# Performance work log

Measured on AMD Instinct MI355X. Metric: run time of the kernel, lower is better.

## Reference

```python
import jax, jax.numpy as jnp
import numpy as np

H, I, E, TOPK = 1024, 4096, 8, 2
B, S = 2, 2048


def setup_inputs() -> dict:
    key = jax.random.key(0)
    ks = jax.random.split(key, 6)
    x = jax.random.normal(ks[0], (B, S, H), dtype=jnp.float32)
    expert_indices = jax.random.randint(ks[1], (B, S, TOPK), 0, E)
    expert_weights = jax.random.uniform(ks[2], (B, S, TOPK), dtype=jnp.float32)
    gate_proj = jax.random.normal(ks[3], (E, I, H), dtype=jnp.float32) * 0.02
    up_proj = jax.random.normal(ks[4], (E, I, H), dtype=jnp.float32) * 0.02
    down_proj = jax.random.normal(ks[5], (E, H, I), dtype=jnp.float32) * 0.02
    return {"x": x, "expert_indices": expert_indices, "expert_weights": expert_weights,
            "gate_proj": gate_proj, "up_proj": up_proj, "down_proj": down_proj}


def reference(x, expert_indices, expert_weights, gate_proj, up_proj, down_proj):
    b, s, h = x.shape
    xf = x.reshape(-1, h)                      # [T, H]
    ei = expert_indices.reshape(-1, expert_indices.shape[-1])   # [T, K]
    ew = expert_weights.reshape(-1, expert_weights.shape[-1])   # [T, K]
    n_experts = gate_proj.shape[0]
    out = jnp.zeros_like(xf)
    for e in range(n_experts):
        # combined routing weight of this expert per token (sum over topk slots)
        w_e = jnp.sum(jnp.where(ei == e, ew, 0.0), axis=-1)     # [T]
        g = xf @ gate_proj[e].T                # [T, I]
        u = xf @ up_proj[e].T                  # [T, I]
        inter = jax.nn.silu(g) * u             # fused SiLU*mul
        out = out + w_e[:, None] * (inter @ down_proj[e].T)     # weighted scatter-add
    return out.reshape(b, s, h)
```

## Files before the change

### kernel.cpp

```cpp
#include <hip/hip_runtime.h>
#include <cstdint>
#include <cstddef>

#define H_DIM 1024
#define I_DIM 4096
#define E_NUM 8
#define TOPK  2
#define T_NUM 4096
#define NROWS (T_NUM * TOPK)
#define BK    64

typedef _Float16 half8 __attribute__((ext_vector_type(8)));
typedef float    f32x4 __attribute__((ext_vector_type(4)));

__device__ __forceinline__ void async_copy16(void* lds, const void* g)
{
    __builtin_amdgcn_global_load_lds(
        (__attribute__((address_space(1))) unsigned int*)g,
        (__attribute__((address_space(3))) unsigned int*)lds,
        16 , 0 , 0 );
}


#define NX4 (T_NUM * H_DIM / 4)
#define NW4 (E_NUM * I_DIM * H_DIM / 4)
__global__ void cvt_all(const float* __restrict__ x,  const float* __restrict__ gp,
                        const float* __restrict__ up, const float* __restrict__ dp,
                        _Float16* __restrict__ xh, _Float16* __restrict__ wg,
                        _Float16* __restrict__ wu, _Float16* __restrict__ wd)
{
    int i = blockIdx.x * blockDim.x + threadIdx.x;
    const int total = NX4 + 3 * NW4;
    if (i >= total) return;
    const float* s; _Float16* d; int j;
    if (i < NX4)              { s = x;  d = xh; j = i; }
    else if (i < NX4 + NW4)   { s = gp; d = wg; j = i - NX4; }
    else if (i < NX4 + 2*NW4) { s = up; d = wu; j = i - NX4 - NW4; }
    else                      { s = dp; d = wd; j = i - NX4 - 2*NW4; }
    float4 v = reinterpret_cast<const float4*>(s)[j];
    union { _Float16 h[4]; unsigned long long u; } o;
    o.h[0] = (_Float16)v.x; o.h[1] = (_Float16)v.y;
    o.h[2] = (_Float16)v.z; o.h[3] = (_Float16)v.w;
    reinterpret_cast<unsigned long long*>(d)[j] = o.u;
}

__global__ void route_all(const int* __restrict__ ei, const float* __restrict__ ew,
                          int* __restrict__ offs,
                          int* __restrict__ token_of_row, float* __restrict__ weight_of_row)
{
    __shared__ int cnt[E_NUM];
    __shared__ int cur[E_NUM];
    const int t = (int)threadIdx.x;
    if (t < E_NUM) cnt[t] = 0;
    __syncthreads();
    for (int s = t; s < NROWS; s += (int)blockDim.x) atomicAdd(&cnt[ei[s]], 1);
    __syncthreads();
    if (t == 0) {
        int acc = 0;
        for (int e = 0; e < E_NUM; ++e) { offs[e] = acc; cur[e] = acc; acc += cnt[e]; }
        offs[E_NUM] = acc;
    }
    __syncthreads();
    for (int s = t; s < NROWS; s += (int)blockDim.x) {
        int e = ei[s];
        int r = atomicAdd(&cur[e], 1);
        token_of_row[r]  = s >> 1;
        weight_of_row[r] = ew[s];
    }
}

__global__ __launch_bounds__(256, 3) void gateup_gemm(
    const _Float16* __restrict__ xh,
    const _Float16* __restrict__ Wg,
    const _Float16* __restrict__ Wu,
    const int*      __restrict__ token_of_row,
    const int*      __restrict__ offs,
    _Float16*       __restrict__ inter)
{
    const int e = blockIdx.z;
    const int seg_start = offs[e], seg_end = offs[e + 1];
    const int m0 = seg_start + (int)blockIdx.y * 128;
    if (m0 >= seg_end) return;
    const int n0 = (int)blockIdx.x * 64;

    __shared__ _Float16 Ash[128 * BK];
    __shared__ _Float16 Bgs[64 * BK];
    __shared__ _Float16 Bus[64 * BK];

    const int tid  = (int)threadIdx.x;
    const int lane = tid & 63, wid = tid >> 6;
    const int wm = wid >> 1, wn = wid & 1;

    const int r8 = lane >> 3;
    const int c8 = lane & 7;
    const int gc = c8 ^ r8;

    const _Float16* pA[4];
    _Float16* lA[4];
#pragma unroll
    for (int j = 0; j < 4; ++j) {
        int q = 4 * wid + j;
        int r = m0 + q * 8 + r8;
        if (r > seg_end - 1) r = seg_end - 1;
        int tok = token_of_row[r];
        pA[j] = xh + (size_t)tok * H_DIM + gc * 8;
        lA[j] = &Ash[q * 8 * BK];
    }
    const _Float16* pBg[2]; const _Float16* pBu[2];
    _Float16* lBg[2]; _Float16* lBu[2];
#pragma unroll
    for (int j = 0; j < 2; ++j) {
        int q = 2 * wid + j;
        int row = q * 8 + r8;
        pBg[j] = Wg + ((size_t)e * I_DIM + n0 + row) * H_DIM + gc * 8;
        pBu[j] = Wu + ((size_t)e * I_DIM + n0 + row) * H_DIM + gc * 8;
        lBg[j] = &Bgs[q * 8 * BK];
        lBu[j] = &Bus[q * 8 * BK];
    }

    f32x4 accg[4][2], accu[4][2];
#pragma unroll
    for (int i = 0; i < 4; ++i)
#pragma unroll
        for (int j = 0; j < 2; ++j) {
            accg[i][j] = (f32x4){0.f, 0.f, 0.f, 0.f};
            accu[i][j] = (f32x4){0.f, 0.f, 0.f, 0.f};
        }

    const int fm = lane & 15, kq = lane >> 4;
    const int f3 = fm & 7;

    constexpr int NK = H_DIM / BK;
    for (int kt = 0; kt < NK; ++kt) {
        const int ko = kt * BK;
        __syncthreads();
#pragma unroll
        for (int j = 0; j < 4; ++j) async_copy16(lA[j], pA[j] + ko);
#pragma unroll
        for (int j = 0; j < 2; ++j) {
            async_copy16(lBg[j], pBg[j] + ko);
            async_copy16(lBu[j], pBu[j] + ko);
        }
        __syncthreads();

#pragma unroll
        for (int h = 0; h < 2; ++h) {
            const int rdo = (((h << 2) | kq) ^ f3) * 8;
            half8 a[4], bg[2], bu[2];
#pragma unroll
            for (int i = 0; i < 4; ++i)
                a[i] = *(const half8*)&Ash[(wm * 64 + i * 16 + fm) * BK + rdo];
#pragma unroll
            for (int j = 0; j < 2; ++j) {
                bg[j] = *(const half8*)&Bgs[(wn * 32 + j * 16 + fm) * BK + rdo];
                bu[j] = *(const half8*)&Bus[(wn * 32 + j * 16 + fm) * BK + rdo];
            }
#pragma unroll
            for (int i = 0; i < 4; ++i)
#pragma unroll
                for (int j = 0; j < 2; ++j) {
                    accg[i][j] = __builtin_amdgcn_mfma_f32_16x16x32_f16(a[i], bg[j], accg[i][j], 0, 0, 0);
                    accu[i][j] = __builtin_amdgcn_mfma_f32_16x16x32_f16(a[i], bu[j], accu[i][j], 0, 0, 0);
                }
        }
    }

#pragma unroll
    for (int i = 0; i < 4; ++i) {
#pragma unroll
        for (int reg = 0; reg < 4; ++reg) {
            int r = m0 + wm * 64 + i * 16 + kq * 4 + reg;
            if (r < seg_end) {
#pragma unroll
                for (int j = 0; j < 2; ++j) {
                    int col = n0 + wn * 32 + j * 16 + fm;
                    float g = accg[i][j][reg];
                    float u = accu[i][j][reg];
                    float sv = (g / (1.f + __expf(-g))) * u;
                    inter[(size_t)r * I_DIM + col] = (_Float16)sv;
                }
            }
        }
    }
}

__global__ __launch_bounds__(256, 3) void down_gemm(
    const _Float16* __restrict__ inter,
    const _Float16* __restrict__ Wd,
    const int*      __restrict__ token_of_row,
    const float*    __restrict__ weight_of_row,
    const int*      __restrict__ offs,
    float*          __restrict__ out)
{
    const int e = blockIdx.z;
    const int seg_start = offs[e], seg_end = offs[e + 1];
    const int m0 = seg_start + (int)blockIdx.y * 128;
    if (m0 >= seg_end) return;
    const int n0 = (int)blockIdx.x * 128;

    __shared__ _Float16 Ash[128 * BK];
    __shared__ _Float16 Bsh[128 * BK];

    const int tid  = (int)threadIdx.x;
    const int lane = tid & 63, wid = tid >> 6;
    const int wm = wid >> 1, wn = wid & 1;
    const int r8 = lane >> 3;
    const int c8 = lane & 7;
    const int gc = c8 ^ r8;

    const _Float16* pA[4]; _Float16* lA[4];
    const _Float16* pB[4]; _Float16* lB[4];
#pragma unroll
    for (int j = 0; j < 4; ++j) {
        int q = 4 * wid + j;
        int row_in = q * 8 + r8;
        int r = m0 + row_in;
        if (r > seg_end - 1) r = seg_end - 1;
        pA[j] = inter + (size_t)r * I_DIM + gc * 8;
        lA[j] = &Ash[q * 8 * BK];
        int n = n0 + row_in;
        pB[j] = Wd + ((size_t)e * H_DIM + n) * I_DIM + gc * 8;
        lB[j] = &Bsh[q * 8 * BK];
    }

    f32x4 acc[4][4];
#pragma unroll
    for (int i = 0; i < 4; ++i)
#pragma unroll
        for (int j = 0; j < 4; ++j) acc[i][j] = (f32x4){0.f, 0.f, 0.f, 0.f};

    const int fm = lane & 15, kq = lane >> 4;
    const int f3 = fm & 7;

    constexpr int NK = I_DIM / BK;
    for (int kt = 0; kt < NK; ++kt) {
        const int ko = kt * BK;
        __syncthreads();
#pragma unroll
        for (int j = 0; j < 4; ++j) {
            async_copy16(lA[j], pA[j] + ko);
            async_copy16(lB[j], pB[j] + ko);
        }
        __syncthreads();

#pragma unroll
        for (int h = 0; h < 2; ++h) {
            const int rdo = (((h << 2) | kq) ^ f3) * 8;
            half8 a[4], b[4];
#pragma unroll
            for (int i = 0; i < 4; ++i)
                a[i] = *(const half8*)&Ash[(wm * 64 + i * 16 + fm) * BK + rdo];
#pragma unroll
            for (int j = 0; j < 4; ++j)
                b[j] = *(const half8*)&Bsh[(wn * 64 + j * 16 + fm) * BK + rdo];
#pragma unroll
            for (int i = 0; i < 4; ++i)
#pragma unroll
                for (int j = 0; j < 4; ++j)
                    acc[i][j] = __builtin_amdgcn_mfma_f32_16x16x32_f16(a[i], b[j], acc[i][j], 0, 0, 0);
        }
    }

#pragma unroll
    for (int i = 0; i < 4; ++i) {
#pragma unroll
        for (int reg = 0; reg < 4; ++reg) {
            int r = m0 + wm * 64 + i * 16 + kq * 4 + reg;
            if (r < seg_end) {
                float w = weight_of_row[r];
                int   t = token_of_row[r];
#pragma unroll
                for (int j = 0; j < 4; ++j) {
                    int col = n0 + wn * 64 + j * 16 + fm;
                    atomicAdd(&out[(size_t)t * H_DIM + col], w * acc[i][j][reg]);
                }
            }
        }
    }
}

extern "C" void kernel_launch(void* const* d_in, const int* in_sizes, int n_in,
                              void* d_out, int out_size, void* d_ws, size_t ws_size,
                              hipStream_t stream)
{
    const float* x  = (const float*)d_in[0];
    const int*   ei = (const int*)  d_in[1];
    const float* ew = (const float*)d_in[2];
    const float* gp = (const float*)d_in[3];
    const float* up = (const float*)d_in[4];
    const float* dp = (const float*)d_in[5];
    float* out = (float*)d_out;

    char* ws = (char*)d_ws;
    size_t o = 0;
    _Float16* xh    = (_Float16*)(ws + o); o += (size_t)T_NUM * H_DIM * 2;
    _Float16* Wg_h  = (_Float16*)(ws + o); o += (size_t)E_NUM * I_DIM * H_DIM * 2;
    _Float16* Wu_h  = (_Float16*)(ws + o); o += (size_t)E_NUM * I_DIM * H_DIM * 2;
    _Float16* Wd_h  = (_Float16*)(ws + o); o += (size_t)E_NUM * I_DIM * H_DIM * 2;
    _Float16* inter = (_Float16*)(ws + o); o += (size_t)NROWS * I_DIM * 2;
    int*   offs          = (int*)  (ws + o);
    int*   token_of_row  = (int*)  (ws + o + 256);
    float* weight_of_row = (float*)(ws + o + 256 + (size_t)NROWS * 4);
    size_t ws_need = o + 256 + (size_t)NROWS * 8;
    if (ws_size < ws_need) return;

    hipMemsetAsync(d_out, 0, (size_t)out_size * sizeof(float), stream);

    const int nt = 256;
    const int ncvt = NX4 + 3 * NW4;
    cvt_all<<<(ncvt + nt - 1) / nt, nt, 0, stream>>>(x, gp, up, dp, xh, Wg_h, Wu_h, Wd_h);

    route_all<<<1, 1024, 0, stream>>>(ei, ew, offs, token_of_row, weight_of_row);

    gateup_gemm<<<dim3(I_DIM / 64, NROWS / 128, E_NUM), 256, 0, stream>>>(
        xh, Wg_h, Wu_h, token_of_row, offs, inter);
    down_gemm<<<dim3(H_DIM / 128, NROWS / 128, E_NUM), 256, 0, stream>>>(
        inter, Wd_h, token_of_row, weight_of_row, offs, out);
}
```

Before: 685.9 us.

## Persistent-style M loops in MoE GEMMs, 512-thread gate/up tiles, fold output zeroing

The gate/up GEMM now uses 512 threads with 256-row M tiles, and each block loops over M tiles with a fixed y-grid instead of launching one block per worst-case tile. The down GEMM gets a similar grid-stride loop over M tiles with a fixed y extent. The conversion kernel becomes grid-stride with 2048 blocks and also zeroes the output, replacing the separate memset. The intent is to cut the many empty blocks launched for the worst-case row count, raise B-tile reuse, and drop one launch. The risks are load imbalance across the fixed y-blocks and lower occupancy from the larger blocks and shared memory.

```diff
diff --git a/kernel.cpp b/kernel.cpp
--- a/kernel.cpp
+++ b/kernel.cpp
@@ -27,21 +27,25 @@
 __global__ void cvt_all(const float* __restrict__ x,  const float* __restrict__ gp,
                         const float* __restrict__ up, const float* __restrict__ dp,
                         _Float16* __restrict__ xh, _Float16* __restrict__ wg,
-                        _Float16* __restrict__ wu, _Float16* __restrict__ wd)
-{
-    int i = blockIdx.x * blockDim.x + threadIdx.x;
+                        _Float16* __restrict__ wu, _Float16* __restrict__ wd,
+                        float* __restrict__ out)
+{
     const int total = NX4 + 3 * NW4;
-    if (i >= total) return;
-    const float* s; _Float16* d; int j;
-    if (i < NX4)              { s = x;  d = xh; j = i; }
-    else if (i < NX4 + NW4)   { s = gp; d = wg; j = i - NX4; }
-    else if (i < NX4 + 2*NW4) { s = up; d = wu; j = i - NX4 - NW4; }
-    else                      { s = dp; d = wd; j = i - NX4 - 2*NW4; }
-    float4 v = reinterpret_cast<const float4*>(s)[j];
-    union { _Float16 h[4]; unsigned long long u; } o;
-    o.h[0] = (_Float16)v.x; o.h[1] = (_Float16)v.y;
-    o.h[2] = (_Float16)v.z; o.h[3] = (_Float16)v.w;
-    reinterpret_cast<unsigned long long*>(d)[j] = o.u;
+    const int nth = (int)(gridDim.x * blockDim.x);
+    for (int i = (int)(blockIdx.x * blockDim.x + threadIdx.x); i < total; i += nth) {
+        const float* s; _Float16* d; int j;
+        if (i < NX4)              { s = x;  d = xh; j = i; }
+        else if (i < NX4 + NW4)   { s = gp; d = wg; j = i - NX4; }
+        else if (i < NX4 + 2*NW4) { s = up; d = wu; j = i - NX4 - NW4; }
+        else                      { s = dp; d = wd; j = i - NX4 - 2*NW4; }
+        float4 v = reinterpret_cast<const float4*>(s)[j];
+        union { _Float16 h[4]; unsigned long long u; } o;
+        o.h[0] = (_Float16)v.x; o.h[1] = (_Float16)v.y;
+        o.h[2] = (_Float16)v.z; o.h[3] = (_Float16)v.w;
+        reinterpret_cast<unsigned long long*>(d)[j] = o.u;
+    }
+    for (int i = (int)(blockIdx.x * blockDim.x + threadIdx.x); i < T_NUM * H_DIM / 4; i += nth)
+        reinterpret_cast<float4*>(out)[i] = (float4){0.f, 0.f, 0.f, 0.f};
 }
 
 __global__ void route_all(const int* __restrict__ ei, const float* __restrict__ ew,
@@ -69,7 +73,8 @@
     }
 }
 
-__global__ __launch_bounds__(256, 3) void gateup_gemm(
+#define GUP_Y 6
+__global__ __launch_bounds__(512) void gateup_gemm(
     const _Float16* __restrict__ xh,
     const _Float16* __restrict__ Wg,
     const _Float16* __restrict__ Wu,
@@ -79,11 +84,9 @@
 {
     const int e = blockIdx.z;
     const int seg_start = offs[e], seg_end = offs[e + 1];
-    const int m0 = seg_start + (int)blockIdx.y * 128;
-    if (m0 >= seg_end) return;
     const int n0 = (int)blockIdx.x * 64;
 
-    __shared__ _Float16 Ash[128 * BK];
+    __shared__ _Float16 Ash[256 * BK];
     __shared__ _Float16 Bgs[64 * BK];
     __shared__ _Float16 Bus[64 * BK];
 
@@ -95,95 +98,89 @@
     const int c8 = lane & 7;
     const int gc = c8 ^ r8;
 
-    const _Float16* pA[4];
-    _Float16* lA[4];
-#pragma unroll
-    for (int j = 0; j < 4; ++j) {
-        int q = 4 * wid + j;
-        int r = m0 + q * 8 + r8;
-        if (r > seg_end - 1) r = seg_end - 1;
-        int tok = token_of_row[r];
-        pA[j] = xh + (size_t)tok * H_DIM + gc * 8;
-        lA[j] = &Ash[q * 8 * BK];
-    }
-    const _Float16* pBg[2]; const _Float16* pBu[2];
-    _Float16* lBg[2]; _Float16* lBu[2];
-#pragma unroll
-    for (int j = 0; j < 2; ++j) {
-        int q = 2 * wid + j;
-        int row = q * 8 + r8;
-        pBg[j] = Wg + ((size_t)e * I_DIM + n0 + row) * H_DIM + gc * 8;
-        pBu[j] = Wu + ((size_t)e * I_DIM + n0 + row) * H_DIM + gc * 8;
-        lBg[j] = &Bgs[q * 8 * BK];
-        lBu[j] = &Bus[q * 8 * BK];
-    }
-
-    f32x4 accg[4][2], accu[4][2];
-#pragma unroll
-    for (int i = 0; i < 4; ++i)
-#pragma unroll
-        for (int j = 0; j < 2; ++j) {
-            accg[i][j] = (f32x4){0.f, 0.f, 0.f, 0.f};
-            accu[i][j] = (f32x4){0.f, 0.f, 0.f, 0.f};
-        }
-
     const int fm = lane & 15, kq = lane >> 4;
     const int f3 = fm & 7;
 
-    constexpr int NK = H_DIM / BK;
-    for (int kt = 0; kt < NK; ++kt) {
-        const int ko = kt * BK;
-        __syncthreads();
-#pragma unroll
-        for (int j = 0; j < 4; ++j) async_copy16(lA[j], pA[j] + ko);
-#pragma unroll
-        for (int j = 0; j < 2; ++j) {
-            async_copy16(lBg[j], pBg[j] + ko);
-            async_copy16(lBu[j], pBu[j] + ko);
-        }
-        __syncthreads();
-
-#pragma unroll
-        for (int h = 0; h < 2; ++h) {
-            const int rdo = (((h << 2) | kq) ^ f3) * 8;
-            half8 a[4], bg[2], bu[2];
-#pragma unroll
-            for (int i = 0; i < 4; ++i)
-                a[i] = *(const half8*)&Ash[(wm * 64 + i * 16 + fm) * BK + rdo];
+    for (int yb = (int)blockIdx.y; seg_start + yb * 256 < seg_end; yb += GUP_Y) {
+        const int m0 = seg_start + yb * 256;
+
+        const _Float16* pA[4]; int oA[4];
+#pragma unroll
+        for (int j = 0; j < 4; ++j) {
+            int q = 4 * wid + j;
+            int r = m0 + q * 8 + r8;
+            if (r > seg_end - 1) r = seg_end - 1;
+            int tok = token_of_row[r];
+            pA[j] = xh + (size_t)tok * H_DIM + gc * 8;
+            oA[j] = q * 8 * BK;
+        }
+        const int brow = wid * 8 + r8;
+        const _Float16* pBg = Wg + ((size_t)e * I_DIM + n0 + brow) * H_DIM + gc * 8;
+        const _Float16* pBu = Wu + ((size_t)e * I_DIM + n0 + brow) * H_DIM + gc * 8;
+        const int oB = wid * 8 * BK;
+
+        f32x4 accg[4][2], accu[4][2];
+#pragma unroll
+        for (int i = 0; i < 4; ++i)
 #pragma unroll
             for (int j = 0; j < 2; ++j) {
-                bg[j] = *(const half8*)&Bgs[(wn * 32 + j * 16 + fm) * BK + rdo];
-                bu[j] = *(const half8*)&Bus[(wn * 32 + j * 16 + fm) * BK + rdo];
-            }
-#pragma unroll
-            for (int i = 0; i < 4; ++i)
+                accg[i][j] = (f32x4){0.f, 0.f, 0.f, 0.f};
+                accu[i][j] = (f32x4){0.f, 0.f, 0.f, 0.f};
+            }
+
+        constexpr int NK = H_DIM / BK;
+        for (int kt = 0; kt < NK; ++kt) {
+            const int ko = kt * BK;
+            __syncthreads();
+#pragma unroll
+            for (int j = 0; j < 4; ++j) async_copy16(&Ash[oA[j]], pA[j] + ko);
+            async_copy16(&Bgs[oB], pBg + ko);
+            async_copy16(&Bus[oB], pBu + ko);
+            __syncthreads();
+
+#pragma unroll
+            for (int h = 0; h < 2; ++h) {
+                const int rdo = (((h << 2) | kq) ^ f3) * 8;
+                half8 a[4], bg[2], bu[2];
+#pragma unroll
+                for (int i = 0; i < 4; ++i)
+                    a[i] = *(const half8*)&Ash[(wm * 64 + i * 16 + fm) * BK + rdo];
 #pragma unroll
                 for (int j = 0; j < 2; ++j) {
-                    accg[i][j] = __builtin_amdgcn_mfma_f32_16x16x32_f16(a[i], bg[j], accg[i][j], 0, 0, 0);
-                    accu[i][j] = __builtin_amdgcn_mfma_f32_16x16x32_f16(a[i], bu[j], accu[i][j], 0, 0, 0);
+                    bg[j] = *(const half8*)&Bgs[(wn * 32 + j * 16 + fm) * BK + rdo];
+                    bu[j] = *(const half8*)&Bus[(wn * 32 + j * 16 + fm) * BK + rdo];
                 }
-        }
-    }
-
-#pragma unroll
-    for (int i = 0; i < 4; ++i) {
-#pragma unroll
-        for (int reg = 0; reg < 4; ++reg) {
-            int r = m0 + wm * 64 + i * 16 + kq * 4 + reg;
-            if (r < seg_end) {
-#pragma unroll
-                for (int j = 0; j < 2; ++j) {
-                    int col = n0 + wn * 32 + j * 16 + fm;
-                    float g = accg[i][j][reg];
-                    float u = accu[i][j][reg];
-                    float sv = (g / (1.f + __expf(-g))) * u;
-                    inter[(size_t)r * I_DIM + col] = (_Float16)sv;
+#pragma unroll
+                for (int i = 0; i < 4; ++i)
+#pragma unroll
+                    for (int j = 0; j < 2; ++j) {
+                        accg[i][j] = __builtin_amdgcn_mfma_f32_16x16x32_f16(a[i], bg[j], accg[i][j], 0, 0, 0);
+                        accu[i][j] = __builtin_amdgcn_mfma_f32_16x16x32_f16(a[i], bu[j], accu[i][j], 0, 0, 0);
+                    }
+            }
+        }
+
+#pragma unroll
+        for (int i = 0; i < 4; ++i) {
+#pragma unroll
+            for (int reg = 0; reg < 4; ++reg) {
+                int r = m0 + wm * 64 + i * 16 + kq * 4 + reg;
+                if (r < seg_end) {
+#pragma unroll
+                    for (int j = 0; j < 2; ++j) {
+                        int col = n0 + wn * 32 + j * 16 + fm;
+                        float g = accg[i][j][reg];
+                        float u = accu[i][j][reg];
+                        float sv = (g / (1.f + __expf(-g))) * u;
+                        inter[(size_t)r * I_DIM + col] = (_Float16)sv;
+                    }
                 }
             }
         }
     }
 }
 
+#define DWN_Y 12
 __global__ __launch_bounds__(256, 3) void down_gemm(
     const _Float16* __restrict__ inter,
     const _Float16* __restrict__ Wd,
@@ -194,8 +191,6 @@
 {
     const int e = blockIdx.z;
     const int seg_start = offs[e], seg_end = offs[e + 1];
-    const int m0 = seg_start + (int)blockIdx.y * 128;
-    if (m0 >= seg_end) return;
     const int n0 = (int)blockIdx.x * 128;
 
     __shared__ _Float16 Ash[128 * BK];
@@ -207,72 +202,75 @@
     const int r8 = lane >> 3;
     const int c8 = lane & 7;
     const int gc = c8 ^ r8;
-
-    const _Float16* pA[4]; _Float16* lA[4];
-    const _Float16* pB[4]; _Float16* lB[4];
-#pragma unroll
-    for (int j = 0; j < 4; ++j) {
-        int q = 4 * wid + j;
-        int row_in = q * 8 + r8;
-        int r = m0 + row_in;
-        if (r > seg_end - 1) r = seg_end - 1;
-        pA[j] = inter + (size_t)r * I_DIM + gc * 8;
-        lA[j] = &Ash[q * 8 * BK];
-        int n = n0 + row_in;
-        pB[j] = Wd + ((size_t)e * H_DIM + n) * I_DIM + gc * 8;
-        lB[j] = &Bsh[q * 8 * BK];
-    }
-
-    f32x4 acc[4][4];
-#pragma unroll
-    for (int i = 0; i < 4; ++i)
-#pragma unroll
-        for (int j = 0; j < 4; ++j) acc[i][j] = (f32x4){0.f, 0.f, 0.f, 0.f};
-
     const int fm = lane & 15, kq = lane >> 4;
     const int f3 = fm & 7;
 
-    constexpr int NK = I_DIM / BK;
-    for (int kt = 0; kt < NK; ++kt) {
-        const int ko = kt * BK;
-        __syncthreads();
+    for (int yb = (int)blockIdx.y; seg_start + yb * 128 < seg_end; yb += DWN_Y) {
+        const int m0 = seg_start + yb * 128;
+
+        const _Float16* pA[4]; int oA[4];
+        const _Float16* pB[4]; int oB[4];
 #pragma unroll
         for (int j = 0; j < 4; ++j) {
-            async_copy16(lA[j], pA[j] + ko);
-            async_copy16(lB[j], pB[j] + ko);
-        }
-        __syncthreads();
-
-#pragma unroll
-        for (int h = 0; h < 2; ++h) {
-            const int rdo = (((h << 2) | kq) ^ f3) * 8;
-            half8 a[4], b[4];
-#pragma unroll
-            for (int i = 0; i < 4; ++i)
-                a[i] = *(const half8*)&Ash[(wm * 64 + i * 16 + fm) * BK + rdo];
-#pragma unroll
-            for (int j = 0; j < 4; ++j)
-                b[j] = *(const half8*)&Bsh[(wn * 64 + j * 16 + fm) * BK + rdo];
-#pragma unroll
-            for (int i = 0; i < 4; ++i)
+            int q = 4 * wid + j;
+            int row_in = q * 8 + r8;
+            int r = m0 + row_in;
+            if (r > seg_end - 1) r = seg_end - 1;
+            pA[j] = inter + (size_t)r * I_DIM + gc * 8;
+            oA[j] = q * 8 * BK;
+            int n = n0 + row_in;
+            pB[j] = Wd + ((size_t)e * H_DIM + n) * I_DIM + gc * 8;
+            oB[j] = q * 8 * BK;
+        }
+
+        f32x4 acc[4][4];
+#pragma unroll
+        for (int i = 0; i < 4; ++i)
+#pragma unroll
+            for (int j = 0; j < 4; ++j) acc[i][j] = (f32x4){0.f, 0.f, 0.f, 0.f};
+
+        constexpr int NK = I_DIM / BK;
+        for (int kt = 0; kt < NK; ++kt) {
+            const int ko = kt * BK;
+            __syncthreads();
+#pragma unroll
+            for (int j = 0; j < 4; ++j) {
+                async_copy16(&Ash[oA[j]], pA[j] + ko);
+                async_copy16(&Bsh[oB[j]], pB[j] + ko);
+            }
+            __syncthreads();
+
+#pragma unroll
+            for (int h = 0; h < 2; ++h) {
+                const int rdo = (((h << 2) | kq) ^ f3) * 8;
+                half8 a[4], b[4];
+#pragma unroll
+                for (int i = 0; i < 4; ++i)
+                    a[i] = *(const half8*)&Ash[(wm * 64 + i * 16 + fm) * BK + rdo];
 #pragma unroll
                 for (int j = 0; j < 4; ++j)
-                    acc[i][j] = __builtin_amdgcn_mfma_f32_16x16x32_f16(a[i], b[j], acc[i][j], 0, 0, 0);
-        }
-    }
-
-#pragma unroll
-    for (int i = 0; i < 4; ++i) {
-#pragma unroll
-        for (int reg = 0; reg < 4; ++reg) {
-            int r = m0 + wm * 64 + i * 16 + kq * 4 + reg;
-            if (r < seg_end) {
-                float w = weight_of_row[r];
-                int   t = token_of_row[r];
-#pragma unroll
-                for (int j = 0; j < 4; ++j) {
-                    int col = n0 + wn * 64 + j * 16 + fm;
-                    atomicAdd(&out[(size_t)t * H_DIM + col], w * acc[i][j][reg]);
+                    b[j] = *(const half8*)&Bsh[(wn * 64 + j * 16 + fm) * BK + rdo];
+#pragma unroll
+                for (int i = 0; i < 4; ++i)
+#pragma unroll
+                    for (int j = 0; j < 4; ++j)
+                        acc[i][j] = __builtin_amdgcn_mfma_f32_16x16x32_f16(a[i], b[j], acc[i][j], 0, 0, 0);
+            }
+        }
+
+#pragma unroll
+        for (int i = 0; i < 4; ++i) {
+#pragma unroll
+            for (int reg = 0; reg < 4; ++reg) {
+                int r = m0 + wm * 64 + i * 16 + kq * 4 + reg;
+                if (r < seg_end) {
+                    float w = weight_of_row[r];
+                    int   t = token_of_row[r];
+#pragma unroll
+                    for (int j = 0; j < 4; ++j) {
+                        int col = n0 + wn * 64 + j * 16 + fm;
+                        atomicAdd(&out[(size_t)t * H_DIM + col], w * acc[i][j][reg]);
+                    }
                 }
             }
         }
@@ -304,16 +302,12 @@
     size_t ws_need = o + 256 + (size_t)NROWS * 8;
     if (ws_size < ws_need) return;
 
-    hipMemsetAsync(d_out, 0, (size_t)out_size * sizeof(float), stream);
-
-    const int nt = 256;
-    const int ncvt = NX4 + 3 * NW4;
-    cvt_all<<<(ncvt + nt - 1) / nt, nt, 0, stream>>>(x, gp, up, dp, xh, Wg_h, Wu_h, Wd_h);
+    cvt_all<<<2048, 256, 0, stream>>>(x, gp, up, dp, xh, Wg_h, Wu_h, Wd_h, out);
 
     route_all<<<1, 1024, 0, stream>>>(ei, ew, offs, token_of_row, weight_of_row);
 
-    gateup_gemm<<<dim3(I_DIM / 64, NROWS / 128, E_NUM), 256, 0, stream>>>(
+    gateup_gemm<<<dim3(I_DIM / 64, GUP_Y, E_NUM), 512, 0, stream>>>(
         xh, Wg_h, Wu_h, token_of_row, offs, inter);
-    down_gemm<<<dim3(H_DIM / 128, NROWS / 128, E_NUM), 256, 0, stream>>>(
+    down_gemm<<<dim3(H_DIM / 128, DWN_Y, E_NUM), 256, 0, stream>>>(
         inter, Wd_h, token_of_row, weight_of_row, offs, out);
 }
```

Result: slower. 778.7 us (+13.5%).
